# Optimization experiments

Measured on AMD Instinct MI355X. Metric: run time of the kernel, lower is better.

Reference implementation:

```python
import jax, jax.numpy as jnp
import numpy as np

N_NODES = 100000
N_EDGES = 1600000
D = 128
L = 3


def setup_inputs() -> dict:
    key = jax.random.key(0)
    k1, k2, k3, k4, k5 = jax.random.split(key, 5)
    x = jax.random.normal(k1, (N_NODES, D), dtype=jnp.float32)
    edge_index = jax.random.randint(k2, (2, N_EDGES), 0, N_NODES, dtype=jnp.int64)
    # Stacked per-layer params (all layers are [D, D] since in==out)
    Wl = jax.random.normal(k3, (L, D, D), dtype=jnp.float32) * 0.05  # lin_l (neighbors), with bias
    bl = jax.random.normal(k4, (L, D), dtype=jnp.float32) * 0.05
    Wr = jax.random.normal(k5, (L, D, D), dtype=jnp.float32) * 0.05  # lin_r (root), no bias
    return {"x": x, "edge_index": edge_index, "Wl": Wl, "bl": bl, "Wr": Wr}


def _sage_conv(x, src, dst, W_l, b_l, W_r):
    # mean aggregation of source features onto target nodes
    msgs = x[src]                                             # [E, D] gather
    agg = jax.ops.segment_sum(msgs, dst, num_segments=N_NODES)  # [N, D] scatter-add
    cnt = jax.ops.segment_sum(jnp.ones((src.shape[0],), x.dtype), dst,
                              num_segments=N_NODES)
    mean = agg / jnp.maximum(cnt, 1.0)[:, None]
    # out = lin_l(mean_neighbors) + lin_r(x)
    return mean @ W_l.T + b_l + x @ W_r.T


def reference(x, edge_index, Wl, bl, Wr):
    src, dst = edge_index[0], edge_index[1]
    for i in range(L):
        x = _sage_conv(x, src, dst, Wl[i], bl[i], Wr[i])
        if i != L - 1:
            x = jax.nn.relu(x)
            # dropout p=0.5 is identity in eval mode
    return jnp.min(x, axis=0)  # [D]
```

## Files before the change

kernel.cpp:

```cpp
#include <hip/hip_runtime.h>
#include <hip/hip_bf16.h>

#define D 128
#define SCAN_C 512
#define BKT 512
#define BKT_SHIFT 9
#define CH 256
#define NBMAX 512
#define MREP 64

typedef __attribute__((ext_vector_type(8))) short bf16x8;
typedef __attribute__((ext_vector_type(4))) float f32x4;

__device__ __forceinline__ float bf16_to_f(unsigned int u) {
    union { unsigned int i; float f; } c; c.i = u << 16; return c.f;
}
__device__ __forceinline__ unsigned short f_to_bf16(float f) {
    union { float f; unsigned int i; } c; c.f = f;
    unsigned int r = c.i + 0x7FFFu + ((c.i >> 16) & 1u);
    return (unsigned short)(r >> 16);
}

__global__ void detect_kernel(const unsigned short* __restrict__ xr,
                              const int* __restrict__ er, int* __restrict__ flag) {
    int plaus = 0;
    for (int i = 0; i < 64; ++i) {
        unsigned short u = xr[2 * i];
        int e = (u >> 7) & 0xFF;
        if (e >= 0x74 && e <= 0x82) plaus++;
    }
    flag[1] = (plaus >= 32) ? 1 : 0;
    int zeros = 0;
    for (int i = 1; i < 128; i += 2) zeros += (er[i] == 0);
    flag[0] = (zeros >= 60) ? 1 : 0;
}

__device__ __forceinline__ int load_idx(const void* p, long long i, int is64) {
    if (is64) return (int)((const long long*)p)[i];
    return ((const int*)p)[i];
}

__global__ void cvt_x_kernel(const void* __restrict__ src, const int* __restrict__ flag,
                             unsigned short* __restrict__ dst, int n) {
    if (flag[1]) return;
    int i = blockIdx.x * blockDim.x + threadIdx.x;
    int stride = gridDim.x * blockDim.x;
    const float* s = (const float*)src;
    for (; i < n; i += stride) dst[i] = f_to_bf16(s[i]);
}

__global__ void cvt_f_kernel(const void* __restrict__ src, const int* __restrict__ flag,
                             float* __restrict__ dst, int n) {
    int is_bf16 = flag[1];
    int i = blockIdx.x * blockDim.x + threadIdx.x;
    int stride = gridDim.x * blockDim.x;
    if (is_bf16) {
        const unsigned short* s = (const unsigned short*)src;
        for (; i < n; i += stride) dst[i] = bf16_to_f(s[i]);
    } else {
        const float* s = (const float*)src;
        for (; i < n; i += stride) dst[i] = s[i];
    }
}

__global__ void packW_kernel(const void* __restrict__ Wl0, const void* __restrict__ Wr0,
                             const int* __restrict__ flag, unsigned short* __restrict__ Wpack,
                             int L) {
    int idx = blockIdx.x * blockDim.x + threadIdx.x;
    if (idx >= L * 8 * 8 * 64) return;
    int lane = idx & 63;
    int ks = (idx >> 6) & 7;
    int nt = (idx >> 9) & 7;
    int layer = idx >> 12;
    int n = nt * 16 + (lane & 15);
    int k0 = ks * 32 + (lane >> 4) * 8;
    int is_bf16 = flag[1];
    unsigned short outv[8];
#pragma unroll
    for (int j = 0; j < 8; ++j) {
        int k = k0 + j;
        size_t off = (size_t)layer * D * D + (size_t)n * D + (k & 127);
        float v;
        if (is_bf16) {
            const unsigned short* W = (const unsigned short*)((k < D) ? Wl0 : Wr0);
            v = bf16_to_f(W[off]);
        } else {
            const float* W = (const float*)((k < D) ? Wl0 : Wr0);
            v = W[off];
        }
        outv[j] = f_to_bf16(v);
    }
    *(uint4*)&Wpack[(size_t)idx * 8] = *(uint4*)outv;
}

__global__ void bucket_hist_kernel(const void* __restrict__ eidx, const int* __restrict__ flag,
                                   int* __restrict__ counts2D, int E, int NB, int EPC) {
    __shared__ int hist[NBMAX];
    int c = blockIdx.x;
    for (int i = threadIdx.x; i < NB; i += blockDim.x) hist[i] = 0;
    __syncthreads();
    int is64 = flag[0];
    int end = min(E, (c + 1) * EPC);
    for (int e = c * EPC + threadIdx.x; e < end; e += blockDim.x) {
        int d = load_idx(eidx, (long long)E + e, is64);
        atomicAdd(&hist[d >> BKT_SHIFT], 1);
    }
    __syncthreads();
    for (int i = threadIdx.x; i < NB; i += blockDim.x)
        counts2D[i * CH + c] = hist[i];
}

__global__ void gscan1_kernel(const int* __restrict__ in, int* __restrict__ blockSums, int n) {
    __shared__ int red[256];
    int base = blockIdx.x * SCAN_C;
    int t = threadIdx.x;
    int s = 0;
    if (base + t < n) s += in[base + t];
    if (base + t + 256 < n) s += in[base + t + 256];
    red[t] = s;
    __syncthreads();
    for (int off = 128; off > 0; off >>= 1) {
        if (t < off) red[t] += red[t + off];
        __syncthreads();
    }
    if (t == 0) blockSums[blockIdx.x] = red[0];
}

__global__ void gscan2_kernel(int* __restrict__ blockSums, int nb) {
    __shared__ int sh[256];
    int t = threadIdx.x;
    int orig = (t < nb) ? blockSums[t] : 0;
    sh[t] = orig;
    __syncthreads();
    for (int off = 1; off < 256; off <<= 1) {
        int v = (t >= off) ? sh[t - off] : 0;
        __syncthreads();
        sh[t] += v;
        __syncthreads();
    }
    if (t < nb) blockSums[t] = sh[t] - orig;
}

__global__ void gscan3_kernel(const int* __restrict__ in, const int* __restrict__ blockBase,
                              int* __restrict__ out, int n) {
    __shared__ int sh[SCAN_C];
    int base = blockIdx.x * SCAN_C;
    int t = threadIdx.x;
    int v0 = (base + t < n) ? in[base + t] : 0;
    int v1 = (base + t + 256 < n) ? in[base + t + 256] : 0;
    sh[t] = v0;
    sh[t + 256] = v1;
    __syncthreads();
    for (int off = 1; off < SCAN_C; off <<= 1) {
        int a = (t >= off) ? sh[t - off] : 0;
        int b = (t + 256 >= off) ? sh[t + 256 - off] : 0;
        __syncthreads();
        sh[t] += a;
        sh[t + 256] += b;
        __syncthreads();
    }
    int bb = blockBase[blockIdx.x];
    if (base + t < n) out[base + t] = bb + sh[t] - v0;
    if (base + t + 256 < n) out[base + t + 256] = bb + sh[t + 256] - v1;
}

__global__ void bucket_scatter_kernel(const void* __restrict__ eidx, const int* __restrict__ flag,
                                      const int* __restrict__ bases2D, unsigned int* __restrict__ ebuf,
                                      int E, int NB, int EPC) {
    __shared__ int cur[NBMAX];
    int c = blockIdx.x;
    for (int i = threadIdx.x; i < NB; i += blockDim.x) cur[i] = bases2D[i * CH + c];
    __syncthreads();
    int is64 = flag[0];
    int end = min(E, (c + 1) * EPC);
    for (int e = c * EPC + threadIdx.x; e < end; e += blockDim.x) {
        int s = load_idx(eidx, e, is64);
        int d = load_idx(eidx, (long long)E + e, is64);
        int b = d >> BKT_SHIFT;
        int pos = atomicAdd(&cur[b], 1);
        ebuf[pos] = ((unsigned)s << BKT_SHIFT) | (unsigned)(d & (BKT - 1));
    }
}

__global__ __launch_bounds__(BKT)
void bucket_csr_kernel(const unsigned int* __restrict__ ebuf, const int* __restrict__ bases2D,
                       int* __restrict__ offsets, int* __restrict__ srcs, int E, int N, int NB) {
    __shared__ int lcnt[BKT];
    __shared__ int sh[BKT];
    __shared__ int lcur[BKT];
    int b = blockIdx.x;
    int t = threadIdx.x;
    int start = bases2D[b * CH];
    int end = (b + 1 < NB) ? bases2D[(b + 1) * CH] : E;
    lcnt[t] = 0;
    __syncthreads();
    for (int e = start + t; e < end; e += BKT)
        atomicAdd(&lcnt[ebuf[e] & (BKT - 1)], 1);
    __syncthreads();
    sh[t] = lcnt[t];
    __syncthreads();
    for (int off = 1; off < BKT; off <<= 1) {
        int v = (t >= off) ? sh[t - off] : 0;
        __syncthreads();
        sh[t] += v;
        __syncthreads();
    }
    int excl = sh[t] - lcnt[t];
    int node = b * BKT + t;
    if (node < N) offsets[node] = start + excl;
    lcur[t] = start + excl;
    __syncthreads();
    for (int e = start + t; e < end; e += BKT) {
        unsigned int p = ebuf[e];
        int pos = atomicAdd(&lcur[p & (BKT - 1)], 1);
        srcs[pos] = (int)(p >> BKT_SHIFT);
    }
    if (b == 0 && t == 0) offsets[N] = E;
}

__global__ void agg_kernel(const unsigned short* __restrict__ xmain,
                           const unsigned short* __restrict__ xalt,
                           const int* __restrict__ flag, const int* __restrict__ offsets,
                           const int* __restrict__ srcs, unsigned short* __restrict__ meanb, int N) {
    const unsigned short* xb = flag[1] ? xalt : xmain;
    int g = blockIdx.x * blockDim.x + threadIdx.x;
    int node = g >> 4;
    int lane = g & 15;
    if (node >= N) return;
    int beg = offsets[node], end = offsets[node + 1];
    float acc[8];
#pragma unroll
    for (int i = 0; i < 8; ++i) acc[i] = 0.f;
    const uint4* xp = (const uint4*)xb;

#define ACC8(v)                                                              \
    acc[0] += bf16_to_f((v).x & 0xFFFFu); acc[1] += bf16_to_f((v).x >> 16);  \
    acc[2] += bf16_to_f((v).y & 0xFFFFu); acc[3] += bf16_to_f((v).y >> 16);  \
    acc[4] += bf16_to_f((v).z & 0xFFFFu); acc[5] += bf16_to_f((v).z >> 16);  \
    acc[6] += bf16_to_f((v).w & 0xFFFFu); acc[7] += bf16_to_f((v).w >> 16);

    int j = beg;
    for (; j + 7 < end; j += 8) {
        int s0 = srcs[j];     int s1 = srcs[j + 1];
        int s2 = srcs[j + 2]; int s3 = srcs[j + 3];
        int s4 = srcs[j + 4]; int s5 = srcs[j + 5];
        int s6 = srcs[j + 6]; int s7 = srcs[j + 7];
        uint4 v0 = xp[(size_t)s0 * 16 + lane];
        uint4 v1 = xp[(size_t)s1 * 16 + lane];
        uint4 v2 = xp[(size_t)s2 * 16 + lane];
        uint4 v3 = xp[(size_t)s3 * 16 + lane];
        uint4 v4 = xp[(size_t)s4 * 16 + lane];
        uint4 v5 = xp[(size_t)s5 * 16 + lane];
        uint4 v6 = xp[(size_t)s6 * 16 + lane];
        uint4 v7 = xp[(size_t)s7 * 16 + lane];
        ACC8(v0); ACC8(v1); ACC8(v2); ACC8(v3);
        ACC8(v4); ACC8(v5); ACC8(v6); ACC8(v7);
    }
    if (j + 3 < end) {
        int s0 = srcs[j];     int s1 = srcs[j + 1];
        int s2 = srcs[j + 2]; int s3 = srcs[j + 3];
        uint4 v0 = xp[(size_t)s0 * 16 + lane];
        uint4 v1 = xp[(size_t)s1 * 16 + lane];
        uint4 v2 = xp[(size_t)s2 * 16 + lane];
        uint4 v3 = xp[(size_t)s3 * 16 + lane];
        ACC8(v0); ACC8(v1); ACC8(v2); ACC8(v3);
        j += 4;
    }
    for (; j < end; ++j) {
        uint4 v = xp[(size_t)srcs[j] * 16 + lane];
        ACC8(v);
    }
#undef ACC8

    float inv = (end > beg) ? 1.0f / (float)(end - beg) : 0.0f;
    uint4 o;
    o.x = (unsigned)f_to_bf16(acc[0] * inv) | ((unsigned)f_to_bf16(acc[1] * inv) << 16);
    o.y = (unsigned)f_to_bf16(acc[2] * inv) | ((unsigned)f_to_bf16(acc[3] * inv) << 16);
    o.z = (unsigned)f_to_bf16(acc[4] * inv) | ((unsigned)f_to_bf16(acc[5] * inv) << 16);
    o.w = (unsigned)f_to_bf16(acc[6] * inv) | ((unsigned)f_to_bf16(acc[7] * inv) << 16);
    ((uint4*)meanb)[(size_t)node * 16 + lane] = o;
}

__global__ __launch_bounds__(512)
void gemm_mfma_kernel(const unsigned short* __restrict__ meanb,
                      const unsigned short* __restrict__ xmain,
                      const unsigned short* __restrict__ xalt,
                      const int* __restrict__ flag,
                      const unsigned short* __restrict__ Wpack, const float* __restrict__ bl,
                      unsigned short* __restrict__ outb, unsigned int* __restrict__ minbuf,
                      int N, int relu, int do_min) {
    __shared__ unsigned short Wlds[8 * 8 * 64 * 8];
    __shared__ float smin[8][D];
    const unsigned short* xb = flag[1] ? xalt : xmain;

    const int tid = threadIdx.x;
    const int wave = tid >> 6;
    const int lane = tid & 63;
    const int m16 = lane & 15;
    const int quad = lane >> 4;
    const int node0 = blockIdx.x * 128;
    const int arow = node0 + wave * 16 + m16;
    const bool rvalid = arow < N;

    {
        const uint4* wsrc = (const uint4*)Wpack;
        uint4* wdst = (uint4*)Wlds;
#pragma unroll
        for (int i = 0; i < 8; ++i) wdst[tid + i * 512] = wsrc[tid + i * 512];
    }
    __syncthreads();

    f32x4 acc[8];
#pragma unroll
    for (int i = 0; i < 8; ++i) acc[i] = (f32x4)0.0f;

#pragma unroll
    for (int ks = 0; ks < 8; ++ks) {
        uint4 tmp = make_uint4(0u, 0u, 0u, 0u);
        if (rvalid) {
            const unsigned short* base = (ks < 4)
                ? meanb + (size_t)arow * D + ks * 32 + quad * 8
                : xb    + (size_t)arow * D + (ks - 4) * 32 + quad * 8;
            tmp = *(const uint4*)base;
        }
        bf16x8 afrag = *(bf16x8*)&tmp;
#pragma unroll
        for (int nt = 0; nt < 8; ++nt) {
            bf16x8 bfrag = *(const bf16x8*)&Wlds[((nt * 8 + ks) * 64 + lane) * 8];
            acc[nt] = __builtin_amdgcn_mfma_f32_16x16x32_bf16(afrag, bfrag, acc[nt], 0, 0, 0);
        }
    }

    if (do_min) {
#pragma unroll
        for (int nt = 0; nt < 8; ++nt) {
            int n = nt * 16 + m16;
            float b = bl[n];
            float m = 3.402823466e38f;
#pragma unroll
            for (int r = 0; r < 4; ++r) {
                int node = node0 + wave * 16 + quad * 4 + r;
                float v = (node < N) ? (acc[nt][r] + b) : 3.402823466e38f;
                m = fminf(m, v);
            }
            m = fminf(m, __shfl_xor(m, 16, 64));
            m = fminf(m, __shfl_xor(m, 32, 64));
            if (quad == 0) smin[wave][n] = m;
        }
        __syncthreads();
        if (tid < D) {
            float m = smin[0][tid];
#pragma unroll
            for (int w = 1; w < 8; ++w) m = fminf(m, smin[w][tid]);
            unsigned bits = __float_as_uint(m);
            unsigned enc = ((int)bits >= 0) ? (bits ^ 0x80000000u) : ~bits;
            atomicMin(&minbuf[(blockIdx.x & (MREP - 1)) * D + tid], enc);
        }
        return;
    }

    __syncthreads();
    {
        unsigned short (*Ot)[136] = (unsigned short (*)[136])Wlds;
#pragma unroll
        for (int nt = 0; nt < 8; ++nt) {
            int n = nt * 16 + m16;
            float b = bl[n];
#pragma unroll
            for (int r = 0; r < 4; ++r) {
                int m = wave * 16 + quad * 4 + r;
                float v = acc[nt][r] + b;
                if (relu) v = fmaxf(v, 0.f);
                Ot[m][n] = f_to_bf16(v);
            }
        }
        __syncthreads();
        for (int i = tid; i < 128 * 16; i += 512) {
            int row = i >> 4;
            int c = i & 15;
            int n = node0 + row;
            if (n < N) ((uint4*)outb)[(size_t)n * 16 + c] = *(uint4*)&Ot[row][c * 8];
        }
    }
}

__global__ void min_out_kernel(const unsigned int* __restrict__ minbuf,
                               const int* __restrict__ flag, void* __restrict__ out) {
    __shared__ unsigned int sh[4][D];
    int tid = threadIdx.x;
    int q = tid >> 7;
    int c = tid & 127;
    unsigned u = 0xFFFFFFFFu;
    for (int r = q; r < MREP; r += 4) u = min(u, minbuf[r * D + c]);
    sh[q][c] = u;
    __syncthreads();
    if (tid < D) {
        unsigned m = min(min(sh[0][tid], sh[1][tid]), min(sh[2][tid], sh[3][tid]));
        unsigned i = (m & 0x80000000u) ? (m ^ 0x80000000u) : ~m;
        union { unsigned i; float f; } cv; cv.i = i;
        if (flag[1]) ((unsigned short*)out)[tid] = f_to_bf16(cv.f);
        else         ((float*)out)[tid] = cv.f;
    }
}

extern "C" void kernel_launch(void* const* d_in, const int* in_sizes, int n_in,
                              void* d_out, int out_size, void* d_ws, size_t ws_size,
                              hipStream_t stream) {
    const void* x0   = d_in[0];
    const void* eidx = d_in[1];
    const void* Wl0  = d_in[2];
    const void* bl0  = d_in[3];
    const void* Wr0  = d_in[4];

    const int N = in_sizes[0] / D;
    const int E = in_sizes[1] / 2;
    const int L = in_sizes[2] / (D * D);

    char* ws = (char*)d_ws;
    size_t off = 0;
    auto alloc = [&](size_t bytes) -> void* {
        void* p = ws + off;
        off += (bytes + 255) & ~(size_t)255;
        return p;
    };
    unsigned short* xb    = (unsigned short*)alloc((size_t)N * D * 2);
    unsigned short* bufA  = (unsigned short*)alloc((size_t)N * D * 2);
    unsigned short* meanb = (unsigned short*)alloc((size_t)N * D * 2);
    int*   offsets = (int*)alloc((size_t)(N + 1) * sizeof(int));
    int*   srcs    = (int*)alloc((size_t)E * sizeof(int));
    int*   flag    = (int*)alloc(256);
    unsigned short* Wpack = (unsigned short*)alloc((size_t)L * 8 * 8 * 64 * 8 * 2);
    float* blf     = (float*)alloc((size_t)L * D * sizeof(float));
    unsigned int* minbuf = (unsigned int*)alloc((size_t)MREP * D * sizeof(unsigned int));
    (void)ws_size; (void)n_in; (void)out_size;

    const int NB  = (N + BKT - 1) / BKT;
    const int EPC = (E + CH - 1) / CH;
    const int n2  = NB * CH;
    unsigned int* ebuf = (unsigned int*)meanb;
    int* counts2D  = (int*)bufA;
    int* bases2D   = counts2D + n2;
    int* blockSums = bases2D + n2;

    detect_kernel<<<1, 1, 0, stream>>>((const unsigned short*)x0, (const int*)eidx, flag);

    cvt_x_kernel<<<2048, 256, 0, stream>>>(x0, flag, xb, N * D);
    cvt_f_kernel<<<8, 256, 0, stream>>>(bl0, flag, blf, L * D);
    packW_kernel<<<(L * 8 * 8 * 64 + 255) / 256, 256, 0, stream>>>(Wl0, Wr0, flag, Wpack, L);

    hipMemsetAsync(minbuf, 0xFF, (size_t)MREP * D * sizeof(unsigned int), stream);

    bucket_hist_kernel<<<CH, 256, 0, stream>>>(eidx, flag, counts2D, E, NB, EPC);
    const int nb2 = (n2 + SCAN_C - 1) / SCAN_C;
    gscan1_kernel<<<nb2, 256, 0, stream>>>(counts2D, blockSums, n2);
    gscan2_kernel<<<1, 256, 0, stream>>>(blockSums, nb2);
    gscan3_kernel<<<nb2, 256, 0, stream>>>(counts2D, blockSums, bases2D, n2);
    bucket_scatter_kernel<<<CH, 256, 0, stream>>>(eidx, flag, bases2D, ebuf, E, NB, EPC);
    bucket_csr_kernel<<<NB, BKT, 0, stream>>>(ebuf, bases2D, offsets, srcs, E, N, NB);

    const unsigned short* cur     = xb;
    const unsigned short* cur_alt = (const unsigned short*)x0;
    unsigned short* nxt = bufA;
    for (int l = 0; l < L; ++l) {
        int last = (l == L - 1);
        int agg_blocks = (N * 16 + 255) / 256;
        agg_kernel<<<agg_blocks, 256, 0, stream>>>(cur, cur_alt, flag, offsets, srcs, meanb, N);
        gemm_mfma_kernel<<<(N + 127) / 128, 512, 0, stream>>>(
            meanb, cur, cur_alt, flag, Wpack + (size_t)l * 8 * 8 * 64 * 8, blf + (size_t)l * D,
            nxt, minbuf, N, last ? 0 : 1, last);
        cur = nxt; cur_alt = nxt;
        nxt = (nxt == bufA) ? xb : bufA;
    }

    min_out_kernel<<<1, 512, 0, stream>>>(minbuf, flag, (void*)d_out);
}
```

Before: 385.9 us.

## Fuse setup kernels into one launch and replace three-pass scan with single-block scan

```diff
diff --git a/kernel.cpp b/kernel.cpp
--- a/kernel.cpp
+++ b/kernel.cpp
@@ -2,7 +2,6 @@
 #include <hip/hip_bf16.h>
 
 #define D 128
-#define SCAN_C 512
 #define BKT 512
 #define BKT_SHIFT 9
 #define CH 256
@@ -21,147 +20,127 @@
     return (unsigned short)(r >> 16);
 }
 
-__global__ void detect_kernel(const unsigned short* __restrict__ xr,
-                              const int* __restrict__ er, int* __restrict__ flag) {
-    int plaus = 0;
-    for (int i = 0; i < 64; ++i) {
-        unsigned short u = xr[2 * i];
-        int e = (u >> 7) & 0xFF;
-        if (e >= 0x74 && e <= 0x82) plaus++;
-    }
-    flag[1] = (plaus >= 32) ? 1 : 0;
-    int zeros = 0;
-    for (int i = 1; i < 128; i += 2) zeros += (er[i] == 0);
-    flag[0] = (zeros >= 60) ? 1 : 0;
-}
-
 __device__ __forceinline__ int load_idx(const void* p, long long i, int is64) {
     if (is64) return (int)((const long long*)p)[i];
     return ((const int*)p)[i];
 }
 
-__global__ void cvt_x_kernel(const void* __restrict__ src, const int* __restrict__ flag,
-                             unsigned short* __restrict__ dst, int n) {
-    if (flag[1]) return;
-    int i = blockIdx.x * blockDim.x + threadIdx.x;
-    int stride = gridDim.x * blockDim.x;
-    const float* s = (const float*)src;
-    for (; i < n; i += stride) dst[i] = f_to_bf16(s[i]);
-}
-
-__global__ void cvt_f_kernel(const void* __restrict__ src, const int* __restrict__ flag,
-                             float* __restrict__ dst, int n) {
-    int is_bf16 = flag[1];
-    int i = blockIdx.x * blockDim.x + threadIdx.x;
-    int stride = gridDim.x * blockDim.x;
-    if (is_bf16) {
-        const unsigned short* s = (const unsigned short*)src;
-        for (; i < n; i += stride) dst[i] = bf16_to_f(s[i]);
-    } else {
-        const float* s = (const float*)src;
-        for (; i < n; i += stride) dst[i] = s[i];
-    }
-}
-
-__global__ void packW_kernel(const void* __restrict__ Wl0, const void* __restrict__ Wr0,
-                             const int* __restrict__ flag, unsigned short* __restrict__ Wpack,
-                             int L) {
-    int idx = blockIdx.x * blockDim.x + threadIdx.x;
-    if (idx >= L * 8 * 8 * 64) return;
-    int lane = idx & 63;
-    int ks = (idx >> 6) & 7;
-    int nt = (idx >> 9) & 7;
-    int layer = idx >> 12;
-    int n = nt * 16 + (lane & 15);
-    int k0 = ks * 32 + (lane >> 4) * 8;
-    int is_bf16 = flag[1];
-    unsigned short outv[8];
-#pragma unroll
-    for (int j = 0; j < 8; ++j) {
-        int k = k0 + j;
-        size_t off = (size_t)layer * D * D + (size_t)n * D + (k & 127);
-        float v;
+__device__ __forceinline__ void detect_inline(const void* x0, const void* eidx,
+                                              int* is_bf16_out, int* is64_out) {
+    const unsigned short* xr = (const unsigned short*)x0;
+    const int* er = (const int*)eidx;
+    const int lane = threadIdx.x & 63;
+    unsigned short u = xr[2 * lane];
+    int e = (u >> 7) & 0xFF;
+    unsigned long long pm = __ballot(e >= 0x74 && e <= 0x82);
+    *is_bf16_out = (__popcll(pm) >= 32) ? 1 : 0;
+    unsigned long long zm = __ballot(er[1 + 2 * lane] == 0);
+    *is64_out = (__popcll(zm) >= 60) ? 1 : 0;
+}
+
+__global__ __launch_bounds__(256)
+void setup_kernel(const void* __restrict__ x0, const void* __restrict__ eidx,
+                  const void* __restrict__ Wl0, const void* __restrict__ Wr0,
+                  const void* __restrict__ bl0,
+                  int* __restrict__ flag, unsigned short* __restrict__ xb,
+                  float* __restrict__ blf, unsigned short* __restrict__ Wpack,
+                  int* __restrict__ counts2D, unsigned int* __restrict__ minbuf,
+                  int N, int E, int L, int NB, int EPC) {
+    __shared__ int hist[NBMAX];
+    int is_bf16, is64;
+    detect_inline(x0, eidx, &is_bf16, &is64);
+    const int b = blockIdx.x;
+    const int t = threadIdx.x;
+    if (b == 0 && t == 0) { flag[0] = is64; flag[1] = is_bf16; }
+
+    if (b < 2048) {
+        if (!is_bf16) {
+            const float* s = (const float*)x0;
+            const int n = N * D;
+            for (int i = b * 256 + t; i < n; i += 2048 * 256) xb[i] = f_to_bf16(s[i]);
+        }
+        return;
+    }
+    if (b < 2048 + CH) {
+        const int c = b - 2048;
+        for (int i = t; i < NB; i += 256) hist[i] = 0;
+        __syncthreads();
+        const int end = min(E, (c + 1) * EPC);
+        for (int e = c * EPC + t; e < end; e += 256) {
+            int d = load_idx(eidx, (long long)E + e, is64);
+            atomicAdd(&hist[d >> BKT_SHIFT], 1);
+        }
+        __syncthreads();
+        for (int i = t; i < NB; i += 256) counts2D[i * CH + c] = hist[i];
+        return;
+    }
+    if (b == 2048 + CH) {
+        const int n = L * D;
         if (is_bf16) {
-            const unsigned short* W = (const unsigned short*)((k < D) ? Wl0 : Wr0);
-            v = bf16_to_f(W[off]);
+            const unsigned short* s = (const unsigned short*)bl0;
+            for (int i = t; i < n; i += 256) blf[i] = bf16_to_f(s[i]);
         } else {
-            const float* W = (const float*)((k < D) ? Wl0 : Wr0);
-            v = W[off];
-        }
-        outv[j] = f_to_bf16(v);
-    }
-    *(uint4*)&Wpack[(size_t)idx * 8] = *(uint4*)outv;
-}
-
-__global__ void bucket_hist_kernel(const void* __restrict__ eidx, const int* __restrict__ flag,
-                                   int* __restrict__ counts2D, int E, int NB, int EPC) {
-    __shared__ int hist[NBMAX];
-    int c = blockIdx.x;
-    for (int i = threadIdx.x; i < NB; i += blockDim.x) hist[i] = 0;
-    __syncthreads();
-    int is64 = flag[0];
-    int end = min(E, (c + 1) * EPC);
-    for (int e = c * EPC + threadIdx.x; e < end; e += blockDim.x) {
-        int d = load_idx(eidx, (long long)E + e, is64);
-        atomicAdd(&hist[d >> BKT_SHIFT], 1);
-    }
-    __syncthreads();
-    for (int i = threadIdx.x; i < NB; i += blockDim.x)
-        counts2D[i * CH + c] = hist[i];
-}
-
-__global__ void gscan1_kernel(const int* __restrict__ in, int* __restrict__ blockSums, int n) {
-    __shared__ int red[256];
-    int base = blockIdx.x * SCAN_C;
-    int t = threadIdx.x;
+            const float* s = (const float*)bl0;
+            for (int i = t; i < n; i += 256) blf[i] = s[i];
+        }
+        return;
+    }
+    if (b == 2048 + CH + 1) {
+        for (int i = t; i < MREP * D; i += 256) minbuf[i] = 0xFFFFFFFFu;
+        return;
+    }
+    {
+        int idx = (b - (2048 + CH + 2)) * 256 + t;
+        if (idx >= L * 8 * 8 * 64) return;
+        int lane = idx & 63;
+        int ks = (idx >> 6) & 7;
+        int nt = (idx >> 9) & 7;
+        int layer = idx >> 12;
+        int n = nt * 16 + (lane & 15);
+        int k0 = ks * 32 + (lane >> 4) * 8;
+        unsigned short outv[8];
+#pragma unroll
+        for (int j = 0; j < 8; ++j) {
+            int k = k0 + j;
+            size_t off = (size_t)layer * D * D + (size_t)n * D + (k & 127);
+            float v;
+            if (is_bf16) {
+                const unsigned short* W = (const unsigned short*)((k < D) ? Wl0 : Wr0);
+                v = bf16_to_f(W[off]);
+            } else {
+                const float* W = (const float*)((k < D) ? Wl0 : Wr0);
+                v = W[off];
+            }
+            outv[j] = f_to_bf16(v);
+        }
+        *(uint4*)&Wpack[(size_t)idx * 8] = *(uint4*)outv;
+    }
+}
+
+__global__ __launch_bounds__(1024)
+void scan_kernel(const int* __restrict__ in, int* __restrict__ out, int n) {
+    __shared__ int psum[1024];
+    const int t = threadIdx.x;
+    const int per = (n + 1023) >> 10;
+    const int base = t * per;
     int s = 0;
-    if (base + t < n) s += in[base + t];
-    if (base + t + 256 < n) s += in[base + t + 256];
-    red[t] = s;
-    __syncthreads();
-    for (int off = 128; off > 0; off >>= 1) {
-        if (t < off) red[t] += red[t + off];
-        __syncthreads();
-    }
-    if (t == 0) blockSums[blockIdx.x] = red[0];
-}
-
-__global__ void gscan2_kernel(int* __restrict__ blockSums, int nb) {
-    __shared__ int sh[256];
-    int t = threadIdx.x;
-    int orig = (t < nb) ? blockSums[t] : 0;
-    sh[t] = orig;
-    __syncthreads();
-    for (int off = 1; off < 256; off <<= 1) {
-        int v = (t >= off) ? sh[t - off] : 0;
-        __syncthreads();
-        sh[t] += v;
-        __syncthreads();
-    }
-    if (t < nb) blockSums[t] = sh[t] - orig;
-}
-
-__global__ void gscan3_kernel(const int* __restrict__ in, const int* __restrict__ blockBase,
-                              int* __restrict__ out, int n) {
-    __shared__ int sh[SCAN_C];
-    int base = blockIdx.x * SCAN_C;
-    int t = threadIdx.x;
-    int v0 = (base + t < n) ? in[base + t] : 0;
-    int v1 = (base + t + 256 < n) ? in[base + t + 256] : 0;
-    sh[t] = v0;
-    sh[t + 256] = v1;
-    __syncthreads();
-    for (int off = 1; off < SCAN_C; off <<= 1) {
-        int a = (t >= off) ? sh[t - off] : 0;
-        int b = (t + 256 >= off) ? sh[t + 256 - off] : 0;
-        __syncthreads();
-        sh[t] += a;
-        sh[t + 256] += b;
-        __syncthreads();
-    }
-    int bb = blockBase[blockIdx.x];
-    if (base + t < n) out[base + t] = bb + sh[t] - v0;
-    if (base + t + 256 < n) out[base + t + 256] = bb + sh[t + 256] - v1;
+    for (int i = 0; i < per; ++i) {
+        int idx = base + i;
+        if (idx < n) s += in[idx];
+    }
+    psum[t] = s;
+    __syncthreads();
+    for (int off = 1; off < 1024; off <<= 1) {
+        int v = (t >= off) ? psum[t - off] : 0;
+        __syncthreads();
+        psum[t] += v;
+        __syncthreads();
+    }
+    int run = psum[t] - s;
+    for (int i = 0; i < per; ++i) {
+        int idx = base + i;
+        if (idx < n) { int v = in[idx]; out[idx] = run; run += v; }
+    }
 }
 
 __global__ void bucket_scatter_kernel(const void* __restrict__ eidx, const int* __restrict__ flag,
@@ -432,29 +411,20 @@
     unsigned short* Wpack = (unsigned short*)alloc((size_t)L * 8 * 8 * 64 * 8 * 2);
     float* blf     = (float*)alloc((size_t)L * D * sizeof(float));
     unsigned int* minbuf = (unsigned int*)alloc((size_t)MREP * D * sizeof(unsigned int));
+    int* counts2D  = (int*)alloc((size_t)NBMAX * CH * sizeof(int));
+    int* bases2D   = (int*)alloc((size_t)NBMAX * CH * sizeof(int));
     (void)ws_size; (void)n_in; (void)out_size;
 
     const int NB  = (N + BKT - 1) / BKT;
     const int EPC = (E + CH - 1) / CH;
     const int n2  = NB * CH;
     unsigned int* ebuf = (unsigned int*)meanb;
-    int* counts2D  = (int*)bufA;
-    int* bases2D   = counts2D + n2;
-    int* blockSums = bases2D + n2;
-
-    detect_kernel<<<1, 1, 0, stream>>>((const unsigned short*)x0, (const int*)eidx, flag);
-
-    cvt_x_kernel<<<2048, 256, 0, stream>>>(x0, flag, xb, N * D);
-    cvt_f_kernel<<<8, 256, 0, stream>>>(bl0, flag, blf, L * D);
-    packW_kernel<<<(L * 8 * 8 * 64 + 255) / 256, 256, 0, stream>>>(Wl0, Wr0, flag, Wpack, L);
-
-    hipMemsetAsync(minbuf, 0xFF, (size_t)MREP * D * sizeof(unsigned int), stream);
-
-    bucket_hist_kernel<<<CH, 256, 0, stream>>>(eidx, flag, counts2D, E, NB, EPC);
-    const int nb2 = (n2 + SCAN_C - 1) / SCAN_C;
-    gscan1_kernel<<<nb2, 256, 0, stream>>>(counts2D, blockSums, n2);
-    gscan2_kernel<<<1, 256, 0, stream>>>(blockSums, nb2);
-    gscan3_kernel<<<nb2, 256, 0, stream>>>(counts2D, blockSums, bases2D, n2);
+
+    const int PACKW_BLOCKS = (L * 8 * 8 * 64 + 255) / 256;
+    setup_kernel<<<2048 + CH + 2 + PACKW_BLOCKS, 256, 0, stream>>>(
+        x0, eidx, Wl0, Wr0, bl0, flag, xb, blf, Wpack, counts2D, minbuf, N, E, L, NB, EPC);
+
+    scan_kernel<<<1, 1024, 0, stream>>>(counts2D, bases2D, n2);
     bucket_scatter_kernel<<<CH, 256, 0, stream>>>(eidx, flag, bases2D, ebuf, E, NB, EPC);
     bucket_csr_kernel<<<NB, BKT, 0, stream>>>(ebuf, bases2D, offsets, srcs, E, N, NB);
 
```

New measurement: 458.3 us. 1.19x slower.
